# Optimization experiments

Hardware: AMD Instinct MI355X
Metric: run time of the kernel (lower is better)

## Reference

```python
import jax, jax.numpy as jnp
import numpy as np
import math
from functools import lru_cache

LMAX = 2
MUL = 64
BATCH = 1024
# all parity-allowed paths for lmax=2, in the module's enumeration order
PATHS = [(0,0,0),(0,1,1),(0,2,2),(1,0,1),(1,1,0),(1,1,2),(1,2,1),(2,0,2),(2,1,1),(2,2,0),(2,2,2)]

# ---- CG tensor construction (numpy, float64), faithful port of the torch source ----

def _counts(L):
    return [(a, b, L - a - b) for a in range(L, -1, -1) for b in range(L - a, -1, -1)]

def _dfact(n):
    out = 1
    for k in range(n, 0, -2):
        out *= k
    return out

def _gmom(n):
    return 0.0 if n % 2 == 1 else float(_dfact(n - 1))

@lru_cache(maxsize=None)
def _gram(L):
    c = _counts(L)
    D = len(c)
    G = np.zeros((D, D))
    for i, (a, b, cc) in enumerate(c):
        for j, (a2, b2, c2) in enumerate(c):
            G[i, j] = _gmom(a + a2) * _gmom(b + b2) * _gmom(cc + c2)
    return G

@lru_cache(maxsize=None)
def _laplacian(L):
    cL = _counts(L)
    cS = _counts(L - 2)
    idxS = {t: i for i, t in enumerate(cS)}
    M = np.zeros((len(cS), len(cL)))
    for j, (a, b, c) in enumerate(cL):
        if a >= 2: M[idxS[(a - 2, b, c)], j] += a * (a - 1)
        if b >= 2: M[idxS[(a, b - 2, c)], j] += b * (b - 1)
        if c >= 2: M[idxS[(a, b, c - 2)], j] += c * (c - 1)
    return M

@lru_cache(maxsize=None)
def _harm_basis(L):
    # harmonic basis in monomial coords: null space of Laplacian, whitened by Gaussian Gram
    if L == 0:
        return np.ones((1, 1))
    if L == 1:
        return np.eye(3)
    Delta = _laplacian(L)
    _, s, vh = np.linalg.svd(Delta, full_matrices=True)
    rank = int((s > 1e-12).sum())
    B = vh[rank:].T
    G = _gram(L)
    M = B.T @ G @ B
    ev, evec = np.linalg.eigh(M)
    ev = np.clip(ev, 1e-14, None)
    W = evec @ np.diag(ev ** -0.5) @ evec.T
    return B @ W

@lru_cache(maxsize=None)
def _r2k_lift(l, k):
    # multiply Sym^l polynomial by (x^2+y^2+z^2)^k -> Sym^{l+2k}
    cl = _counts(l)
    cL = _counts(l + 2 * k)
    idxL = {t: i for i, t in enumerate(cL)}
    M = np.zeros((len(cL), len(cl)))
    for i in range(k + 1):
        for j in range(k - i + 1):
            h = k - i - j
            coef = math.factorial(k) / (math.factorial(i) * math.factorial(j) * math.factorial(h))
            for col, (a, b, c) in enumerate(cl):
                M[idxL[(a + 2 * i, b + 2 * j, c + 2 * h)], col] += coef
    return M

@lru_cache(maxsize=None)
def _poly_mult(l1, l2, L):
    c1, c2, cL = _counts(l1), _counts(l2), _counts(L)
    idxL = {t: i for i, t in enumerate(cL)}
    M = np.zeros((len(cL), len(c1) * len(c2)))
    for i, a in enumerate(c1):
        for j, b in enumerate(c2):
            M[idxL[(a[0] + b[0], a[1] + b[1], a[2] + b[2])], i * len(c2) + j] = 1.0
    return M

@lru_cache(maxsize=None)
def _projector(L, l):
    # P_{L->l}: monomial coeffs of Sym^L -> harmonic coords of Harm^l
    k = (L - l) // 2
    GL = _gram(L)
    Bl = _harm_basis(l)
    V = _r2k_lift(l, k) @ Bl
    G = V.T @ GL @ V
    return np.linalg.solve(G, V.T @ GL)

@lru_cache(maxsize=None)
def _cg(l1, l2, l3):
    L = l1 + l2
    P = _projector(L, l3)
    B1, B2 = _harm_basis(l1), _harm_basis(l2)
    Mp = _poly_mult(l1, l2, L)
    m1, m2 = 2 * l1 + 1, 2 * l2 + 1
    outer = np.einsum('im,jn->ijmn', B1, B2).reshape(B1.shape[0] * B2.shape[0], m1 * m2)
    C = (P @ (Mp @ outer)).T.reshape(m1, m2, 2 * l3 + 1)
    n = np.linalg.norm(C)
    if n > 1e-30:  # 'component' normalization
        C = C * (math.sqrt(2 * l3 + 1) / n)
    return C


def setup_inputs() -> dict:
    key = jax.random.key(0)
    ks = jax.random.split(key, 7)
    inp = {}
    for l in range(LMAX + 1):
        inp[f'x1_l{l}'] = jax.random.normal(ks[l], (BATCH, MUL, 2 * l + 1), dtype=jnp.float32)
        inp[f'x2_l{l}'] = jax.random.normal(ks[l + 3], (BATCH, MUL, 2 * l + 1), dtype=jnp.float32)
    inp['W'] = jax.random.normal(ks[6], (len(PATHS), MUL, MUL, MUL), dtype=jnp.float32) * 0.02
    for p, (l1, l2, l3) in enumerate(PATHS):
        inp[f'C_{p}'] = jnp.asarray(_cg(l1, l2, l3), dtype=jnp.float32)
    return inp


def reference(x1_l0, x1_l1, x1_l2, x2_l0, x2_l1, x2_l2, W,
              C_0, C_1, C_2, C_3, C_4, C_5, C_6, C_7, C_8, C_9, C_10):
    x1 = {0: x1_l0, 1: x1_l1, 2: x1_l2}
    x2 = {0: x2_l0, 1: x2_l1, 2: x2_l2}
    Cs = [C_0, C_1, C_2, C_3, C_4, C_5, C_6, C_7, C_8, C_9, C_10]
    B = x1_l0.shape[0]
    mul_out = W.shape[1]
    out = {l: jnp.zeros((B, mul_out, 2 * l + 1), dtype=x1_l0.dtype) for l in range(LMAX + 1)}
    for p, (l1, l2, l3) in enumerate(PATHS):
        # out[z,w,k] += sum_{u,v,m,n} x1[z,u,m] x2[z,v,n] W[p,w,u,v] C[p][m,n,k]
        out[l3] = out[l3] + jnp.einsum('zum,zvn,wuv,mnk->zwk',
                                       x1[l1], x2[l2], W[p], Cs[p], optimize='optimal')
    # concatenate the output irrep dict l -> (B, mul_out, 2l+1) along the m axis
    return jnp.concatenate([out[l] for l in range(LMAX + 1)], axis=-1)
```

## Files before the change

kernel.cpp:

```cpp
#include <hip/hip_runtime.h>


#define NTHREADS 256
#define SMEM_BYTES 32768

typedef __attribute__((ext_vector_type(4))) float f32x4;
typedef __attribute__((ext_vector_type(8))) short s16x8;

__device__ __forceinline__ unsigned short f2bf(float x) {
    __bf16 b = (__bf16)x;
    union { __bf16 h; unsigned short u; } v;
    v.h = b;
    return v.u;
}


__global__ __launch_bounds__(NTHREADS) void prep_w(const float* __restrict__ W,
                                                   unsigned short* __restrict__ Wb)
{
    int id = blockIdx.x * NTHREADS + threadIdx.x;
    int v4 = (id & 15) << 2;
    int w  = (id >> 4) & 63;
    int u  = (id >> 10) & 63;
    int p  = id >> 16;
    float4 f = *(const float4*)(W + (((size_t)p * 64 + w) * 64 + u) * 64 + v4);
    ushort4 h;
    h.x = f2bf(f.x); h.y = f2bf(f.y); h.z = f2bf(f.z); h.w = f2bf(f.w);
    *(ushort4*)(Wb + (((size_t)p * 64 + u) * 64 + w) * 64 + v4) = h;
}


struct KArgs {
    const float*          x1[3];
    const float*          x2[3];
    const unsigned short* Wb;
    const float*          C[11];
    float*                part[11];
};

template <int M1, int N1, int K1, int ZT, int S1, int UC>
__device__ __forceinline__ void run_path(const float* __restrict__ x1g,
                                         const float* __restrict__ x2g,
                                         const unsigned short* __restrict__ Wbp,
                                         const float* __restrict__ Cg,
                                         float* __restrict__ partp,
                                         int local, char* __restrict__ smem)
{
    constexpr int KN   = K1 * N1;
    constexpr int NC   = ZT * K1 / 16;
    constexpr bool EVEN = (NC % 2 == 0);
    constexpr int ROWT = EVEN ? 2 : 1;
    constexpr int COLT = EVEN ? NC / 2 : NC;
    constexpr int NI   = ZT / 4;
    constexpr int SST  = UC * S1 + 4;
    constexpr int TROWS = ZT * K1;

    float*          sC  = (float*)smem;
    float*          sc1 = (float*)(smem + 512);
    unsigned short* sT0 = (unsigned short*)(smem + 512 + ZT * SST * 4);

    const int t = threadIdx.x, lane = t & 63, wave = t >> 6;
    const int ln = lane & 15, q = lane >> 4;
    const int ztile = local >> 2, usub = local & 3;
    const int z0 = ztile * ZT, u0 = usub * 16;

    for (int i = t; i < M1 * N1 * K1; i += NTHREADS) sC[i] = Cg[i];
    __syncthreads();

    auto build_slab = [&](int us0) {
        for (int i = t; i < ZT * UC * KN; i += NTHREADS) {
            int z   = i / (UC * KN);
            int r   = i - z * (UC * KN);
            int uu2 = r / KN;
            int j   = r - uu2 * KN;
            int k   = j / N1, n = j - k * N1;
            const float* x1r = x1g + ((size_t)(z0 + z) * 64 + u0 + us0 + uu2) * M1;
            float s = 0.f;
#pragma unroll
            for (int m = 0; m < M1; ++m) s += x1r[m] * sC[(m * N1 + n) * K1 + k];
            sc1[z * SST + uu2 * S1 + j] = s;
        }
    };

    float xr[NI][N1];
#pragma unroll
    for (int i = 0; i < NI; ++i) {
        const float* xp = x2g + ((size_t)(z0 + i * 4 + wave) * 64 + lane) * N1;
#pragma unroll
        for (int n = 0; n < N1; ++n) xr[i][n] = xp[n];
    }

    auto tform = [&](int uf, unsigned short* sTn) {
        const int uus = uf & (UC - 1);
#pragma unroll
        for (int i = 0; i < NI; ++i) {
            const int z = i * 4 + wave;
            const float4* cp = (const float4*)&sc1[z * SST + uus * S1];
            float c1v[S1];
#pragma unroll
            for (int jj = 0; jj < S1 / 4; ++jj) {
                float4 f = cp[jj];
                c1v[jj * 4 + 0] = f.x; c1v[jj * 4 + 1] = f.y;
                c1v[jj * 4 + 2] = f.z; c1v[jj * 4 + 3] = f.w;
            }
#pragma unroll
            for (int k = 0; k < K1; ++k) {
                float s = 0.f;
#pragma unroll
                for (int n = 0; n < N1; ++n) s += xr[i][n] * c1v[k * N1 + n];
                sTn[(z * K1 + k) * 72 + lane] = f2bf(s);
            }
        }
    };

    f32x4 acc[ROWT][COLT];
#pragma unroll
    for (int rt = 0; rt < ROWT; ++rt)
#pragma unroll
        for (int ci = 0; ci < COLT; ++ci) acc[rt][ci] = (f32x4){0.f, 0.f, 0.f, 0.f};

    build_slab(0);
    __syncthreads();
    tform(0, sT0);
    __syncthreads();

#pragma unroll 2
    for (int uu = 0; uu < 16; ++uu) {
        if (((uu + 1) & (UC - 1)) == 0 && (uu + 1) < 16) {
            build_slab(uu + 1);
            __syncthreads();
        }
        const int cur = uu & 1;
        unsigned short* sTc = sT0 + cur * (TROWS * 72);
        unsigned short* sTn = sT0 + (cur ^ 1) * (TROWS * 72);

        const unsigned short* wsrc = Wbp + (size_t)(u0 + uu) * 4096;
        s16x8 areg[ROWT][2];
#pragma unroll
        for (int rt = 0; rt < ROWT; ++rt) {
            const int wt = EVEN ? ((wave >> 1) * 2 + rt) : wave;
#pragma unroll
            for (int s2 = 0; s2 < 2; ++s2)
                areg[rt][s2] = *(const s16x8*)(wsrc + (wt * 16 + ln) * 64 + s2 * 32 + q * 8);
        }

        if (uu < 15) tform(uu + 1, sTn);

#pragma unroll
        for (int ci = 0; ci < COLT; ++ci) {
            const int c = EVEN ? ((wave & 1) * COLT + ci) : ci;
            s16x8 bf0 = *(const s16x8*)&sTc[(c * 16 + ln) * 72 + q * 8];
            s16x8 bf1 = *(const s16x8*)&sTc[(c * 16 + ln) * 72 + 32 + q * 8];
#pragma unroll
            for (int rt = 0; rt < ROWT; ++rt) {
                acc[rt][ci] = __builtin_amdgcn_mfma_f32_16x16x32_bf16(
                    areg[rt][0], bf0, acc[rt][ci], 0, 0, 0);
                acc[rt][ci] = __builtin_amdgcn_mfma_f32_16x16x32_bf16(
                    areg[rt][1], bf1, acc[rt][ci], 0, 0, 0);
            }
        }
        __syncthreads();
    }

#pragma unroll
    for (int rt = 0; rt < ROWT; ++rt) {
        const int wt = EVEN ? ((wave >> 1) * 2 + rt) : wave;
#pragma unroll
        for (int ci = 0; ci < COLT; ++ci) {
            const int c = EVEN ? ((wave & 1) * COLT + ci) : ci;
            const int col = c * 16 + ln;
            const int z = col / K1, k = col - z * K1;
            float* op = partp + ((size_t)(usub * K1 + k) * 1024 + z0 + z) * 64
                        + wt * 16 + q * 4;
            *(f32x4*)op = acc[rt][ci];
        }
    }
}

__global__ __launch_bounds__(NTHREADS, 5) void tp_main(KArgs a)
{
    __shared__ __align__(16) char smem[SMEM_BYTES];

    const int bid = blockIdx.x;
    const int starts[12] = {0, 256, 512, 768, 1024, 1280, 1408, 1536, 1664, 1792, 1920, 2048};
    int idx = 0;
#pragma unroll
    for (int i = 1; i < 12; ++i) idx += (bid >= starts[i]) ? 1 : 0;
    const int local = bid - starts[idx];

    switch (idx) {
        case 0:  run_path<1,5,5,16,28, 4>(a.x1[0], a.x2[2], a.Wb + (size_t) 2*262144, a.C[2],  a.part[2],  local, smem); break;
        case 1:  run_path<5,5,5,16,28, 4>(a.x1[2], a.x2[2], a.Wb + (size_t)10*262144, a.C[10], a.part[10], local, smem); break;
        case 2:  run_path<3,3,5,16,16, 8>(a.x1[1], a.x2[1], a.Wb + (size_t) 5*262144, a.C[5],  a.part[5],  local, smem); break;
        case 3:  run_path<5,1,5,16, 8,16>(a.x1[2], a.x2[0], a.Wb + (size_t) 7*262144, a.C[7],  a.part[7],  local, smem); break;
        case 4:  run_path<3,5,3,16,16, 8>(a.x1[1], a.x2[2], a.Wb + (size_t) 6*262144, a.C[6],  a.part[6],  local, smem); break;
        case 5:  run_path<1,3,3,32,12, 2>(a.x1[0], a.x2[1], a.Wb + (size_t) 1*262144, a.C[1],  a.part[1],  local, smem); break;
        case 6:  run_path<5,3,3,32,12, 2>(a.x1[2], a.x2[1], a.Wb + (size_t) 8*262144, a.C[8],  a.part[8],  local, smem); break;
        case 7:  run_path<3,1,3,32, 4, 8>(a.x1[1], a.x2[0], a.Wb + (size_t) 3*262144, a.C[3],  a.part[3],  local, smem); break;
        case 8:  run_path<5,5,1,32, 8,16>(a.x1[2], a.x2[2], a.Wb + (size_t) 9*262144, a.C[9],  a.part[9],  local, smem); break;
        case 9:  run_path<3,3,1,32, 4,16>(a.x1[1], a.x2[1], a.Wb + (size_t) 4*262144, a.C[4],  a.part[4],  local, smem); break;
        case 10: run_path<1,1,1,32, 4,16>(a.x1[0], a.x2[0], a.Wb + (size_t) 0*262144, a.C[0],  a.part[0],  local, smem); break;
        default: break;
    }
}


struct RArgs {
    const float* part[11];
    float*       out;
};

__global__ __launch_bounds__(NTHREADS) void reduce_out(RArgs r)
{
    __shared__ float red[3 * 64 * 9];
    const int lane = threadIdx.x & 63, us = threadIdx.x >> 6;
    const int zw = blockIdx.x * 64 + lane;
    const int z = zw >> 6, w = zw & 63;

    float o[9];
#pragma unroll
    for (int i = 0; i < 9; ++i) o[i] = 0.f;

    {
        const int P[3] = {0, 4, 9};
#pragma unroll
        for (int pi = 0; pi < 3; ++pi)
            o[0] += r.part[P[pi]][((size_t)us * 1024 + z) * 64 + w];
    }
    {
        const int P[4] = {1, 3, 6, 8};
#pragma unroll
        for (int pi = 0; pi < 4; ++pi) {
            const float* pp = r.part[P[pi]];
#pragma unroll
            for (int k = 0; k < 3; ++k)
                o[1 + k] += pp[((size_t)(us * 3 + k) * 1024 + z) * 64 + w];
        }
    }
    {
        const int P[4] = {2, 5, 7, 10};
#pragma unroll
        for (int pi = 0; pi < 4; ++pi) {
            const float* pp = r.part[P[pi]];
#pragma unroll
            for (int k = 0; k < 5; ++k)
                o[4 + k] += pp[((size_t)(us * 5 + k) * 1024 + z) * 64 + w];
        }
    }

    if (us > 0) {
#pragma unroll
        for (int i = 0; i < 9; ++i) red[((us - 1) * 64 + lane) * 9 + i] = o[i];
    }
    __syncthreads();
    if (us == 0) {
#pragma unroll
        for (int i = 0; i < 9; ++i)
            o[i] += red[(0 * 64 + lane) * 9 + i]
                  + red[(1 * 64 + lane) * 9 + i]
                  + red[(2 * 64 + lane) * 9 + i];
        float* op = r.out + (size_t)zw * 9;
#pragma unroll
        for (int i = 0; i < 9; ++i) op[i] = o[i];
    }
}


extern "C" void kernel_launch(void* const* d_in, const int* in_sizes, int n_in,
                              void* d_out, int out_size, void* d_ws, size_t ws_size,
                              hipStream_t stream)
{
    static const int cumK1[11] = {0, 1, 4, 9, 12, 13, 18, 21, 26, 29, 30};

    unsigned short* Wb = (unsigned short*)d_ws;
    float* partbase = (float*)((char*)d_ws + (6u << 20));

    KArgs a;
    a.x1[0] = (const float*)d_in[0];
    a.x2[0] = (const float*)d_in[1];
    a.x1[1] = (const float*)d_in[2];
    a.x2[1] = (const float*)d_in[3];
    a.x1[2] = (const float*)d_in[4];
    a.x2[2] = (const float*)d_in[5];
    a.Wb = Wb;
    RArgs rr;
    for (int p = 0; p < 11; ++p) {
        a.C[p]    = (const float*)d_in[7 + p];
        a.part[p] = partbase + (size_t)cumK1[p] * 262144;
        rr.part[p] = a.part[p];
    }
    rr.out = (float*)d_out;

    prep_w<<<dim3(720896 / NTHREADS), NTHREADS, 0, stream>>>((const float*)d_in[6], Wb);
    tp_main<<<dim3(2048), NTHREADS, 0, stream>>>(a);
    reduce_out<<<dim3(1024), NTHREADS, 0, stream>>>(rr);
}
```

Measured before the change: 174.6 us.

## Add double-buffered software-pipelined path kernel for K1=5/3 paths

Introduces run_path2, which double-buffers the bf16 transformed operand tiles in shared memory. Building and transforming the next pair of u slices overlaps with the MFMA accumulation on the current pair, and each wave owns a full 16-row w tile. The first five paths switch to it. Shared memory grows to about 54 KB and launch bounds drop from 5 to 3 blocks per CU, trading occupancy for overlap of the transform work with the matrix instructions.

```diff
diff --git a/kernel.cpp b/kernel.cpp
--- a/kernel.cpp
+++ b/kernel.cpp
@@ -2,7 +2,7 @@
 
 
 #define NTHREADS 256
-#define SMEM_BYTES 32768
+#define SMEM_BYTES 54016
 
 typedef __attribute__((ext_vector_type(4))) float f32x4;
 typedef __attribute__((ext_vector_type(8))) short s16x8;
@@ -38,6 +38,144 @@
     float*                part[11];
 };
 
+template <int M1, int N1, int K1, int ZT, int S1>
+__device__ __forceinline__ void run_path2(const float* __restrict__ x1g,
+                                          const float* __restrict__ x2g,
+                                          const unsigned short* __restrict__ Wbp,
+                                          const float* __restrict__ Cg,
+                                          float* __restrict__ partp,
+                                          int local, char* __restrict__ smem)
+{
+    constexpr int KN    = K1 * N1;
+    constexpr int NC    = ZT * K1 / 16;
+    constexpr int NI    = ZT / 4;
+    constexpr int UC    = 4;
+    constexpr int SST   = UC * S1 + 4;
+    constexpr int TROWS = ZT * K1;
+    constexpr int JSTR  = TROWS * 72;
+    constexpr int BSTR  = 2 * JSTR;
+
+    float*          sC  = (float*)smem;
+    float*          sc1 = (float*)(smem + 512);
+    unsigned short* sT0 = (unsigned short*)(smem + 512 + ZT * SST * 4);
+
+    const int t = threadIdx.x, lane = t & 63, wave = t >> 6;
+    const int ln = lane & 15, q = lane >> 4;
+    const int ztile = local >> 2, usub = local & 3;
+    const int z0 = ztile * ZT, u0 = usub * 16;
+
+    for (int i = t; i < M1 * N1 * K1; i += NTHREADS) sC[i] = Cg[i];
+    __syncthreads();
+
+    auto build2 = [&](int pr) {
+        const int us0 = 2 * pr;
+        const int ub  = us0 & (UC - 1);
+        for (int i = t; i < ZT * 2 * KN; i += NTHREADS) {
+            int z   = i / (2 * KN);
+            int r   = i - z * (2 * KN);
+            int uu2 = r / KN;
+            int j   = r - uu2 * KN;
+            int k   = j / N1, n = j - k * N1;
+            const float* x1r = x1g + ((size_t)(z0 + z) * 64 + u0 + us0 + uu2) * M1;
+            float s = 0.f;
+#pragma unroll
+            for (int m = 0; m < M1; ++m) s += x1r[m] * sC[(m * N1 + n) * K1 + k];
+            sc1[z * SST + (ub + uu2) * S1 + j] = s;
+        }
+    };
+
+    float xr[NI][N1];
+#pragma unroll
+    for (int i = 0; i < NI; ++i) {
+        const float* xp = x2g + ((size_t)(z0 + i * 4 + wave) * 64 + lane) * N1;
+#pragma unroll
+        for (int n = 0; n < N1; ++n) xr[i][n] = xp[n];
+    }
+
+    auto tform = [&](int uf, unsigned short* sTn) {
+        const int uus = uf & (UC - 1);
+#pragma unroll
+        for (int i = 0; i < NI; ++i) {
+            const int z = i * 4 + wave;
+            const float4* cp = (const float4*)&sc1[z * SST + uus * S1];
+            float c1v[S1];
+#pragma unroll
+            for (int jj = 0; jj < S1 / 4; ++jj) {
+                float4 f = cp[jj];
+                c1v[jj * 4 + 0] = f.x; c1v[jj * 4 + 1] = f.y;
+                c1v[jj * 4 + 2] = f.z; c1v[jj * 4 + 3] = f.w;
+            }
+#pragma unroll
+            for (int k = 0; k < K1; ++k) {
+                float s = 0.f;
+#pragma unroll
+                for (int n = 0; n < N1; ++n) s += xr[i][n] * c1v[k * N1 + n];
+                sTn[(z * K1 + k) * 72 + lane] = f2bf(s);
+            }
+        }
+    };
+
+    f32x4 acc[NC];
+#pragma unroll
+    for (int ci = 0; ci < NC; ++ci) acc[ci] = (f32x4){0.f, 0.f, 0.f, 0.f};
+
+    build2(0);
+    build2(1);
+    __syncthreads();
+    tform(0, sT0);
+    tform(1, sT0 + JSTR);
+    __syncthreads();
+
+#pragma unroll 2
+    for (int ph = 0; ph < 8; ++ph) {
+        const int cur = ph & 1;
+        unsigned short* sTc = sT0 + cur * BSTR;
+        unsigned short* sTn = sT0 + (cur ^ 1) * BSTR;
+
+        if (ph + 2 < 8) build2(ph + 2);
+
+        s16x8 areg[2][2];
+#pragma unroll
+        for (int j = 0; j < 2; ++j) {
+            const unsigned short* wsrc = Wbp + (size_t)(u0 + 2 * ph + j) * 4096;
+#pragma unroll
+            for (int s2 = 0; s2 < 2; ++s2)
+                areg[j][s2] = *(const s16x8*)(wsrc + (wave * 16 + ln) * 64 + s2 * 32 + q * 8);
+        }
+
+        if (ph + 1 < 8) {
+            tform(2 * ph + 2, sTn);
+            tform(2 * ph + 3, sTn + JSTR);
+        }
+
+        __builtin_amdgcn_s_setprio(1);
+#pragma unroll
+        for (int ci = 0; ci < NC; ++ci) {
+#pragma unroll
+            for (int j = 0; j < 2; ++j) {
+                const unsigned short* tb = sTc + j * JSTR + (ci * 16 + ln) * 72;
+                s16x8 bf0 = *(const s16x8*)(tb + q * 8);
+                s16x8 bf1 = *(const s16x8*)(tb + 32 + q * 8);
+                acc[ci] = __builtin_amdgcn_mfma_f32_16x16x32_bf16(
+                    areg[j][0], bf0, acc[ci], 0, 0, 0);
+                acc[ci] = __builtin_amdgcn_mfma_f32_16x16x32_bf16(
+                    areg[j][1], bf1, acc[ci], 0, 0, 0);
+            }
+        }
+        __builtin_amdgcn_s_setprio(0);
+        __syncthreads();
+    }
+
+#pragma unroll
+    for (int ci = 0; ci < NC; ++ci) {
+        const int col = ci * 16 + ln;
+        const int z = col / K1, k = col - z * K1;
+        float* op = partp + ((size_t)(usub * K1 + k) * 1024 + z0 + z) * 64
+                    + wave * 16 + q * 4;
+        *(f32x4*)op = acc[ci];
+    }
+}
+
 template <int M1, int N1, int K1, int ZT, int S1, int UC>
 __device__ __forceinline__ void run_path(const float* __restrict__ x1g,
                                          const float* __restrict__ x2g,
@@ -177,7 +315,7 @@
     }
 }
 
-__global__ __launch_bounds__(NTHREADS, 5) void tp_main(KArgs a)
+__global__ __launch_bounds__(NTHREADS, 3) void tp_main(KArgs a)
 {
     __shared__ __align__(16) char smem[SMEM_BYTES];
 
@@ -189,11 +327,11 @@
     const int local = bid - starts[idx];
 
     switch (idx) {
-        case 0:  run_path<1,5,5,16,28, 4>(a.x1[0], a.x2[2], a.Wb + (size_t) 2*262144, a.C[2],  a.part[2],  local, smem); break;
-        case 1:  run_path<5,5,5,16,28, 4>(a.x1[2], a.x2[2], a.Wb + (size_t)10*262144, a.C[10], a.part[10], local, smem); break;
-        case 2:  run_path<3,3,5,16,16, 8>(a.x1[1], a.x2[1], a.Wb + (size_t) 5*262144, a.C[5],  a.part[5],  local, smem); break;
-        case 3:  run_path<5,1,5,16, 8,16>(a.x1[2], a.x2[0], a.Wb + (size_t) 7*262144, a.C[7],  a.part[7],  local, smem); break;
-        case 4:  run_path<3,5,3,16,16, 8>(a.x1[1], a.x2[2], a.Wb + (size_t) 6*262144, a.C[6],  a.part[6],  local, smem); break;
+        case 0:  run_path2<1,5,5,16,28>(a.x1[0], a.x2[2], a.Wb + (size_t) 2*262144, a.C[2],  a.part[2],  local, smem); break;
+        case 1:  run_path2<5,5,5,16,28>(a.x1[2], a.x2[2], a.Wb + (size_t)10*262144, a.C[10], a.part[10], local, smem); break;
+        case 2:  run_path2<3,3,5,16,16>(a.x1[1], a.x2[1], a.Wb + (size_t) 5*262144, a.C[5],  a.part[5],  local, smem); break;
+        case 3:  run_path2<5,1,5,16, 8>(a.x1[2], a.x2[0], a.Wb + (size_t) 7*262144, a.C[7],  a.part[7],  local, smem); break;
+        case 4:  run_path2<3,5,3,16,16>(a.x1[1], a.x2[2], a.Wb + (size_t) 6*262144, a.C[6],  a.part[6],  local, smem); break;
         case 5:  run_path<1,3,3,32,12, 2>(a.x1[0], a.x2[1], a.Wb + (size_t) 1*262144, a.C[1],  a.part[1],  local, smem); break;
         case 6:  run_path<5,3,3,32,12, 2>(a.x1[2], a.x2[1], a.Wb + (size_t) 8*262144, a.C[8],  a.part[8],  local, smem); break;
         case 7:  run_path<3,1,3,32, 4, 8>(a.x1[1], a.x2[0], a.Wb + (size_t) 3*262144, a.C[3],  a.part[3],  local, smem); break;
```

Measured after the change: 193.2 us. +10.7%, slower.

## Restructure tensor-product kernel into single-wave blocks with uniform 16-row z tiles

Applied to the files above, without the earlier changes.

The main kernel moves from 256-thread blocks with per-path z tiles of 16 or 32 to 64-thread single-wave blocks. Each block covers 16 batch rows by 16 u values for one path, which gives 2816 uniform blocks. The double-buffered transform/MFMA overlap is dropped for a simpler build-sync-compute loop, and some paths now reload x2 from global memory instead of keeping it in registers. This is meant to improve load balance and occupancy and to cut block-wide sync cost, but each wave now does all four W row tiles and loses the prefetch overlap.

```diff
diff --git a/kernel.cpp b/kernel.cpp
--- a/kernel.cpp
+++ b/kernel.cpp
@@ -2,7 +2,8 @@
 
 
 #define NTHREADS 256
-#define SMEM_BYTES 32768
+#define TP_THREADS 64
+#define SMEM_BYTES 15872
 
 typedef __attribute__((ext_vector_type(4))) float f32x4;
 typedef __attribute__((ext_vector_type(8))) short s16x8;
@@ -38,37 +39,34 @@
     float*                part[11];
 };
 
-template <int M1, int N1, int K1, int ZT, int S1, int UC>
-__device__ __forceinline__ void run_path(const float* __restrict__ x1g,
-                                         const float* __restrict__ x2g,
-                                         const unsigned short* __restrict__ Wbp,
-                                         const float* __restrict__ Cg,
-                                         float* __restrict__ partp,
-                                         int local, char* __restrict__ smem)
-{
-    constexpr int KN   = K1 * N1;
-    constexpr int NC   = ZT * K1 / 16;
-    constexpr bool EVEN = (NC % 2 == 0);
-    constexpr int ROWT = EVEN ? 2 : 1;
-    constexpr int COLT = EVEN ? NC / 2 : NC;
-    constexpr int NI   = ZT / 4;
-    constexpr int SST  = UC * S1 + 4;
-    constexpr int TROWS = ZT * K1;
+template <int M1, int N1, int K1, int S1, int UC, bool XH>
+__device__ __forceinline__ void run_path1(const float* __restrict__ x1g,
+                                          const float* __restrict__ x2g,
+                                          const unsigned short* __restrict__ Wbp,
+                                          const float* __restrict__ Cg,
+                                          float* __restrict__ partp,
+                                          int local, char* __restrict__ smem)
+{
+    constexpr int KN    = K1 * N1;
+    constexpr int NC    = K1;
+    constexpr int SST   = UC * S1 + 4;
+    constexpr int TROWS = 16 * K1;
+    constexpr int TOT   = 16 * UC * KN;
 
     float*          sC  = (float*)smem;
     float*          sc1 = (float*)(smem + 512);
-    unsigned short* sT0 = (unsigned short*)(smem + 512 + ZT * SST * 4);
-
-    const int t = threadIdx.x, lane = t & 63, wave = t >> 6;
-    const int ln = lane & 15, q = lane >> 4;
+    unsigned short* sT  = (unsigned short*)(smem + 512 + 16 * SST * 4);
+
+    const int t = threadIdx.x;
+    const int ln = t & 15, q = t >> 4;
     const int ztile = local >> 2, usub = local & 3;
-    const int z0 = ztile * ZT, u0 = usub * 16;
-
-    for (int i = t; i < M1 * N1 * K1; i += NTHREADS) sC[i] = Cg[i];
+    const int z0 = ztile * 16, u0 = usub * 16;
+
+    for (int i = t; i < M1 * N1 * K1; i += TP_THREADS) sC[i] = Cg[i];
     __syncthreads();
 
     auto build_slab = [&](int us0) {
-        for (int i = t; i < ZT * UC * KN; i += NTHREADS) {
+        for (int i = t; i < TOT; i += TP_THREADS) {
             int z   = i / (UC * KN);
             int r   = i - z * (UC * KN);
             int uu2 = r / KN;
@@ -82,19 +80,20 @@
         }
     };
 
-    float xr[NI][N1];
-#pragma unroll
-    for (int i = 0; i < NI; ++i) {
-        const float* xp = x2g + ((size_t)(z0 + i * 4 + wave) * 64 + lane) * N1;
-#pragma unroll
-        for (int n = 0; n < N1; ++n) xr[i][n] = xp[n];
-    }
-
-    auto tform = [&](int uf, unsigned short* sTn) {
+    float xr[XH ? 16 : 1][N1];
+    if constexpr (XH) {
+#pragma unroll
+        for (int z = 0; z < 16; ++z) {
+            const float* xp = x2g + ((size_t)(z0 + z) * 64 + t) * N1;
+#pragma unroll
+            for (int n = 0; n < N1; ++n) xr[z][n] = xp[n];
+        }
+    }
+
+    auto tform = [&](int uf) {
         const int uus = uf & (UC - 1);
 #pragma unroll
-        for (int i = 0; i < NI; ++i) {
-            const int z = i * 4 + wave;
+        for (int z = 0; z < 16; ++z) {
             const float4* cp = (const float4*)&sc1[z * SST + uus * S1];
             float c1v[S1];
 #pragma unroll
@@ -103,103 +102,95 @@
                 c1v[jj * 4 + 0] = f.x; c1v[jj * 4 + 1] = f.y;
                 c1v[jj * 4 + 2] = f.z; c1v[jj * 4 + 3] = f.w;
             }
+            float xv[N1];
+            if constexpr (XH) {
+#pragma unroll
+                for (int n = 0; n < N1; ++n) xv[n] = xr[z][n];
+            } else {
+                const float* xp = x2g + ((size_t)(z0 + z) * 64 + t) * N1;
+#pragma unroll
+                for (int n = 0; n < N1; ++n) xv[n] = xp[n];
+            }
 #pragma unroll
             for (int k = 0; k < K1; ++k) {
                 float s = 0.f;
 #pragma unroll
-                for (int n = 0; n < N1; ++n) s += xr[i][n] * c1v[k * N1 + n];
-                sTn[(z * K1 + k) * 72 + lane] = f2bf(s);
+                for (int n = 0; n < N1; ++n) s += xv[n] * c1v[k * N1 + n];
+                sT[(z * K1 + k) * 72 + t] = f2bf(s);
             }
         }
     };
 
-    f32x4 acc[ROWT][COLT];
-#pragma unroll
-    for (int rt = 0; rt < ROWT; ++rt)
-#pragma unroll
-        for (int ci = 0; ci < COLT; ++ci) acc[rt][ci] = (f32x4){0.f, 0.f, 0.f, 0.f};
-
-    build_slab(0);
-    __syncthreads();
-    tform(0, sT0);
-    __syncthreads();
-
-#pragma unroll 2
+    f32x4 acc[4][NC];
+#pragma unroll
+    for (int wt = 0; wt < 4; ++wt)
+#pragma unroll
+        for (int ci = 0; ci < NC; ++ci) acc[wt][ci] = (f32x4){0.f, 0.f, 0.f, 0.f};
+
     for (int uu = 0; uu < 16; ++uu) {
-        if (((uu + 1) & (UC - 1)) == 0 && (uu + 1) < 16) {
-            build_slab(uu + 1);
+        if ((uu & (UC - 1)) == 0) {
+            build_slab(uu);
             __syncthreads();
         }
-        const int cur = uu & 1;
-        unsigned short* sTc = sT0 + cur * (TROWS * 72);
-        unsigned short* sTn = sT0 + (cur ^ 1) * (TROWS * 72);
 
         const unsigned short* wsrc = Wbp + (size_t)(u0 + uu) * 4096;
-        s16x8 areg[ROWT][2];
-#pragma unroll
-        for (int rt = 0; rt < ROWT; ++rt) {
-            const int wt = EVEN ? ((wave >> 1) * 2 + rt) : wave;
+        s16x8 areg[4][2];
+#pragma unroll
+        for (int wt = 0; wt < 4; ++wt)
 #pragma unroll
             for (int s2 = 0; s2 < 2; ++s2)
-                areg[rt][s2] = *(const s16x8*)(wsrc + (wt * 16 + ln) * 64 + s2 * 32 + q * 8);
-        }
-
-        if (uu < 15) tform(uu + 1, sTn);
-
-#pragma unroll
-        for (int ci = 0; ci < COLT; ++ci) {
-            const int c = EVEN ? ((wave & 1) * COLT + ci) : ci;
-            s16x8 bf0 = *(const s16x8*)&sTc[(c * 16 + ln) * 72 + q * 8];
-            s16x8 bf1 = *(const s16x8*)&sTc[(c * 16 + ln) * 72 + 32 + q * 8];
-#pragma unroll
-            for (int rt = 0; rt < ROWT; ++rt) {
-                acc[rt][ci] = __builtin_amdgcn_mfma_f32_16x16x32_bf16(
-                    areg[rt][0], bf0, acc[rt][ci], 0, 0, 0);
-                acc[rt][ci] = __builtin_amdgcn_mfma_f32_16x16x32_bf16(
-                    areg[rt][1], bf1, acc[rt][ci], 0, 0, 0);
-            }
-        }
+                areg[wt][s2] = *(const s16x8*)(wsrc + (wt * 16 + ln) * 64 + s2 * 32 + q * 8);
+
+        tform(uu);
         __syncthreads();
-    }
-
-#pragma unroll
-    for (int rt = 0; rt < ROWT; ++rt) {
-        const int wt = EVEN ? ((wave >> 1) * 2 + rt) : wave;
-#pragma unroll
-        for (int ci = 0; ci < COLT; ++ci) {
-            const int c = EVEN ? ((wave & 1) * COLT + ci) : ci;
-            const int col = c * 16 + ln;
+
+#pragma unroll
+        for (int ci = 0; ci < NC; ++ci) {
+            const unsigned short* tb = sT + (ci * 16 + ln) * 72;
+            s16x8 bf0 = *(const s16x8*)(tb + q * 8);
+            s16x8 bf1 = *(const s16x8*)(tb + 32 + q * 8);
+#pragma unroll
+            for (int wt = 0; wt < 4; ++wt) {
+                acc[wt][ci] = __builtin_amdgcn_mfma_f32_16x16x32_bf16(
+                    areg[wt][0], bf0, acc[wt][ci], 0, 0, 0);
+                acc[wt][ci] = __builtin_amdgcn_mfma_f32_16x16x32_bf16(
+                    areg[wt][1], bf1, acc[wt][ci], 0, 0, 0);
+            }
+        }
+        __syncthreads();
+    }
+
+#pragma unroll
+    for (int wt = 0; wt < 4; ++wt)
+#pragma unroll
+        for (int ci = 0; ci < NC; ++ci) {
+            const int col = ci * 16 + ln;
             const int z = col / K1, k = col - z * K1;
             float* op = partp + ((size_t)(usub * K1 + k) * 1024 + z0 + z) * 64
                         + wt * 16 + q * 4;
-            *(f32x4*)op = acc[rt][ci];
-        }
-    }
-}
-
-__global__ __launch_bounds__(NTHREADS, 5) void tp_main(KArgs a)
+            *(f32x4*)op = acc[wt][ci];
+        }
+}
+
+__global__ __launch_bounds__(TP_THREADS, 2) void tp_main(KArgs a)
 {
     __shared__ __align__(16) char smem[SMEM_BYTES];
 
-    const int bid = blockIdx.x;
-    const int starts[12] = {0, 256, 512, 768, 1024, 1280, 1408, 1536, 1664, 1792, 1920, 2048};
-    int idx = 0;
-#pragma unroll
-    for (int i = 1; i < 12; ++i) idx += (bid >= starts[i]) ? 1 : 0;
-    const int local = bid - starts[idx];
-
-    switch (idx) {
-        case 0:  run_path<1,5,5,16,28, 4>(a.x1[0], a.x2[2], a.Wb + (size_t) 2*262144, a.C[2],  a.part[2],  local, smem); break;
-        case 1:  run_path<5,5,5,16,28, 4>(a.x1[2], a.x2[2], a.Wb + (size_t)10*262144, a.C[10], a.part[10], local, smem); break;
-        case 2:  run_path<3,3,5,16,16, 8>(a.x1[1], a.x2[1], a.Wb + (size_t) 5*262144, a.C[5],  a.part[5],  local, smem); break;
-        case 3:  run_path<5,1,5,16, 8,16>(a.x1[2], a.x2[0], a.Wb + (size_t) 7*262144, a.C[7],  a.part[7],  local, smem); break;
-        case 4:  run_path<3,5,3,16,16, 8>(a.x1[1], a.x2[2], a.Wb + (size_t) 6*262144, a.C[6],  a.part[6],  local, smem); break;
-        case 5:  run_path<1,3,3,32,12, 2>(a.x1[0], a.x2[1], a.Wb + (size_t) 1*262144, a.C[1],  a.part[1],  local, smem); break;
-        case 6:  run_path<5,3,3,32,12, 2>(a.x1[2], a.x2[1], a.Wb + (size_t) 8*262144, a.C[8],  a.part[8],  local, smem); break;
-        case 7:  run_path<3,1,3,32, 4, 8>(a.x1[1], a.x2[0], a.Wb + (size_t) 3*262144, a.C[3],  a.part[3],  local, smem); break;
-        case 8:  run_path<5,5,1,32, 8,16>(a.x1[2], a.x2[2], a.Wb + (size_t) 9*262144, a.C[9],  a.part[9],  local, smem); break;
-        case 9:  run_path<3,3,1,32, 4,16>(a.x1[1], a.x2[1], a.Wb + (size_t) 4*262144, a.C[4],  a.part[4],  local, smem); break;
-        case 10: run_path<1,1,1,32, 4,16>(a.x1[0], a.x2[0], a.Wb + (size_t) 0*262144, a.C[0],  a.part[0],  local, smem); break;
+    const int pi = blockIdx.x >> 8;
+    const int local = blockIdx.x & 255;
+
+    switch (pi) {
+        case 0:  run_path1<1,5,5,28,2,false>(a.x1[0], a.x2[2], a.Wb + (size_t) 2*262144, a.C[2],  a.part[2],  local, smem); break;
+        case 1:  run_path1<5,5,5,28,2,false>(a.x1[2], a.x2[2], a.Wb + (size_t)10*262144, a.C[10], a.part[10], local, smem); break;
+        case 2:  run_path1<3,3,5,16,2,true >(a.x1[1], a.x2[1], a.Wb + (size_t) 5*262144, a.C[5],  a.part[5],  local, smem); break;
+        case 3:  run_path1<5,1,5, 8,2,true >(a.x1[2], a.x2[0], a.Wb + (size_t) 7*262144, a.C[7],  a.part[7],  local, smem); break;
+        case 4:  run_path1<3,5,3,16,2,false>(a.x1[1], a.x2[2], a.Wb + (size_t) 6*262144, a.C[6],  a.part[6],  local, smem); break;
+        case 5:  run_path1<1,3,3,12,2,true >(a.x1[0], a.x2[1], a.Wb + (size_t) 1*262144, a.C[1],  a.part[1],  local, smem); break;
+        case 6:  run_path1<5,3,3,12,2,true >(a.x1[2], a.x2[1], a.Wb + (size_t) 8*262144, a.C[8],  a.part[8],  local, smem); break;
+        case 7:  run_path1<3,1,3, 4,2,true >(a.x1[1], a.x2[0], a.Wb + (size_t) 3*262144, a.C[3],  a.part[3],  local, smem); break;
+        case 8:  run_path1<5,5,1, 8,2,true >(a.x1[2], a.x2[2], a.Wb + (size_t) 9*262144, a.C[9],  a.part[9],  local, smem); break;
+        case 9:  run_path1<3,3,1, 4,2,true >(a.x1[1], a.x2[1], a.Wb + (size_t) 4*262144, a.C[4],  a.part[4],  local, smem); break;
+        case 10: run_path1<1,1,1, 4,2,true >(a.x1[0], a.x2[0], a.Wb + (size_t) 0*262144, a.C[0],  a.part[0],  local, smem); break;
         default: break;
     }
 }
@@ -292,6 +283,6 @@
     rr.out = (float*)d_out;
 
     prep_w<<<dim3(720896 / NTHREADS), NTHREADS, 0, stream>>>((const float*)d_in[6], Wb);
-    tp_main<<<dim3(2048), NTHREADS, 0, stream>>>(a);
+    tp_main<<<dim3(2816), TP_THREADS, 0, stream>>>(a);
     reduce_out<<<dim3(1024), NTHREADS, 0, stream>>>(rr);
 }
```

After: 198.3 us. 13.6% more time.
